# Kernel tuning notes

Measured on AMD Instinct MI355X. Metric: run time of the kernel, lower is better.

## Reference

```python
import jax, jax.numpy as jnp
import numpy as np

N = 50000      # nodes
E = 800000     # edges (before self-loops)
DIN = 128      # in_channels
DH = 64        # hidden_channels
HEADS = 2
DOUT = 64      # out_channels
NEG_SLOPE = 0.2  # PyG GATConv leaky_relu slope


def setup_inputs() -> dict:
    key = jax.random.key(0)
    ks = jax.random.split(key, 10)
    node_emb = jax.random.normal(ks[0], (N, DIN), dtype=jnp.float32)
    edge_index = jax.random.randint(ks[1], (2, E), 0, N, dtype=jnp.int64)
    # conv1: in -> hidden, heads=2, concat=True
    W1 = jax.random.normal(ks[2], (DIN, HEADS * DH), dtype=jnp.float32) / np.sqrt(DIN)
    att_src1 = jax.random.normal(ks[3], (HEADS, DH), dtype=jnp.float32) * 0.1
    att_dst1 = jax.random.normal(ks[4], (HEADS, DH), dtype=jnp.float32) * 0.1
    b1 = jnp.zeros((HEADS * DH,), dtype=jnp.float32)
    # conv2: hidden*heads -> out, heads=1, concat=False
    W2 = jax.random.normal(ks[5], (HEADS * DH, 1 * DOUT), dtype=jnp.float32) / np.sqrt(HEADS * DH)
    att_src2 = jax.random.normal(ks[6], (1, DOUT), dtype=jnp.float32) * 0.1
    att_dst2 = jax.random.normal(ks[7], (1, DOUT), dtype=jnp.float32) * 0.1
    b2 = jnp.zeros((DOUT,), dtype=jnp.float32)
    return {"node_emb": node_emb, "edge_index": edge_index,
            "W1": W1, "att_src1": att_src1, "att_dst1": att_dst1, "b1": b1,
            "W2": W2, "att_src2": att_src2, "att_dst2": att_dst2, "b2": b2}


def gat_layer(x, src, dst, W, att_src, att_dst, bias, heads, concat, n):
    # x: [N, Fin]; W: [Fin, heads*C]; att_*: [heads, C]
    C = W.shape[1] // heads
    h = (x @ W).reshape(n, heads, C)                       # [N, H, C]
    a_src = jnp.einsum('nhc,hc->nh', h, att_src)           # [N, H]
    a_dst = jnp.einsum('nhc,hc->nh', h, att_dst)           # [N, H]
    e = jax.nn.leaky_relu(a_src[src] + a_dst[dst], NEG_SLOPE)  # [E, H]
    # segment softmax over incoming edges of each destination node
    m = jax.ops.segment_max(e, dst, num_segments=n)        # [N, H]
    ex = jnp.exp(e - m[dst])
    denom = jax.ops.segment_sum(ex, dst, num_segments=n)   # [N, H]
    alpha = ex / denom[dst]                                # [E, H]
    out = jax.ops.segment_sum(h[src] * alpha[:, :, None], dst, num_segments=n)  # [N, H, C]
    if concat:
        out = out.reshape(n, heads * C)
    else:
        out = out.mean(axis=1)
    return out + bias


def reference(node_emb, edge_index, W1, att_src1, att_dst1, b1, W2, att_src2, att_dst2, b2):
    loops = jnp.arange(N, dtype=edge_index.dtype)
    src = jnp.concatenate([edge_index[0], loops])  # PyG add_self_loops=True
    dst = jnp.concatenate([edge_index[1], loops])
    h = gat_layer(node_emb, src, dst, W1, att_src1, att_dst1, b1, HEADS, True, N)
    h = jax.nn.elu(h)
    # dropout is identity in eval mode
    out = gat_layer(h, src, dst, W2, att_src2, att_dst2, b2, 1, False, N)
    return out
```

## Files before the change

kernel.cpp:

```cpp
#include <hip/hip_runtime.h>
#include <hip/hip_fp16.h>
#include <math.h>

constexpr float NEG_SLOPE = 0.2f;
constexpr int NPART = 8;
constexpr int WSLOT = 16;

__global__ void k_scatter(const int* __restrict__ src, const int* __restrict__ dst, int e,
                          int* __restrict__ cur, unsigned short* __restrict__ ell, int n) {
    int t = blockIdx.x * blockDim.x + threadIdx.x;
    int i0 = t * 4;
    int p = blockIdx.x & (NPART - 1);
    if (i0 + 3 < e) {
        int4 d4 = *reinterpret_cast<const int4*>(dst + i0);
        int4 s4 = *reinterpret_cast<const int4*>(src + i0);
        int a0 = atomicAdd(&cur[p * n + d4.x], 1);
        int a1 = atomicAdd(&cur[p * n + d4.y], 1);
        int a2 = atomicAdd(&cur[p * n + d4.z], 1);
        int a3 = atomicAdd(&cur[p * n + d4.w], 1);
        if (a0 < WSLOT) ell[((size_t)p * n + d4.x) * WSLOT + a0] = (unsigned short)s4.x;
        if (a1 < WSLOT) ell[((size_t)p * n + d4.y) * WSLOT + a1] = (unsigned short)s4.y;
        if (a2 < WSLOT) ell[((size_t)p * n + d4.z) * WSLOT + a2] = (unsigned short)s4.z;
        if (a3 < WSLOT) ell[((size_t)p * n + d4.w) * WSLOT + a3] = (unsigned short)s4.w;
    } else {
        for (int i = i0; i < e; i++) {
            int d = dst[i];
            int slot = atomicAdd(&cur[p * n + d], 1);
            if (slot < WSLOT) ell[((size_t)p * n + d) * WSLOT + slot] = (unsigned short)src[i];
        }
    }
}

__device__ inline __half2 u2h(unsigned int u) { return *reinterpret_cast<__half2*>(&u); }

__device__ inline void fmamix8(uint4 v, float al, float* acc) {
    float2 f0 = __half22float2(u2h(v.x)), f1 = __half22float2(u2h(v.y));
    float2 f2 = __half22float2(u2h(v.z)), f3 = __half22float2(u2h(v.w));
    acc[0] = fmaf(al, f0.x, acc[0]); acc[1] = fmaf(al, f0.y, acc[1]);
    acc[2] = fmaf(al, f1.x, acc[2]); acc[3] = fmaf(al, f1.y, acc[3]);
    acc[4] = fmaf(al, f2.x, acc[4]); acc[5] = fmaf(al, f2.y, acc[5]);
    acc[6] = fmaf(al, f3.x, acc[6]); acc[7] = fmaf(al, f3.y, acc[7]);
}

__device__ inline int ell_resolve(const unsigned short* __restrict__ ell,
                                  const int* pre, int node, int n, int l) {
    int p = 0;
#pragma unroll
    for (int t = 1; t < NPART; t++)
        if (l >= pre[t]) p = t;
    int slot = l - pre[p];
    return (int)ell[((size_t)p * n + node) * WSLOT + slot];
}

__global__ __launch_bounds__(256) void k_gemm1(const float* __restrict__ x,
                                               const float* __restrict__ W,
                                               const float* __restrict__ a_src,
                                               const float* __restrict__ a_dst,
                                               __half* __restrict__ h1h,
                                               float* __restrict__ att, int n) {
    __shared__ float xs[32 * 128];
    __shared__ float ws[128 * 128];
    int t = threadIdx.x;
    const float4* Wv = (const float4*)W;
    float4* wsv = (float4*)ws;
#pragma unroll
    for (int i = 0; i < 16; i++) wsv[t + 256 * i] = Wv[t + 256 * i];
    int row0 = blockIdx.x * 32;
    const float4* xv = (const float4*)x;
    float4* xsv = (float4*)xs;
#pragma unroll
    for (int ii = 0; ii < 4; ii++) {
        int i = t + 256 * ii;
        int r = i >> 5, c4 = i & 31;
        int gr = row0 + r;
        float4 v = (gr < n) ? xv[(size_t)gr * 32 + c4] : make_float4(0.f, 0.f, 0.f, 0.f);
        xsv[i] = v;
    }
    __syncthreads();
    int tc = t & 31;
    int tr = t >> 5;
    float acc[4][4];
#pragma unroll
    for (int i = 0; i < 4; i++)
#pragma unroll
        for (int j = 0; j < 4; j++) acc[i][j] = 0.f;
    const float4* wsv4 = (const float4*)ws;
    for (int k = 0; k < 128; k++) {
        float4 w4 = wsv4[k * 32 + tc];
#pragma unroll
        for (int i = 0; i < 4; i++) {
            float xvv = xs[(tr * 4 + i) * 128 + k];
            acc[i][0] = fmaf(xvv, w4.x, acc[i][0]);
            acc[i][1] = fmaf(xvv, w4.y, acc[i][1]);
            acc[i][2] = fmaf(xvv, w4.z, acc[i][2]);
            acc[i][3] = fmaf(xvv, w4.w, acc[i][3]);
        }
    }
#pragma unroll
    for (int i = 0; i < 4; i++) {
        int gr = row0 + tr * 4 + i;
        if (gr < n) {
            __half2 p01 = __floats2half2_rn(acc[i][0], acc[i][1]);
            __half2 p23 = __floats2half2_rn(acc[i][2], acc[i][3]);
            uint2 o;
            o.x = *reinterpret_cast<unsigned int*>(&p01);
            o.y = *reinterpret_cast<unsigned int*>(&p23);
            *reinterpret_cast<uint2*>(h1h + (size_t)gr * 128 + 4 * tc) = o;
        }
    }
    const float4* asv = (const float4*)a_src;
    const float4* adv = (const float4*)a_dst;
    float4 as4 = asv[tc], ad4 = adv[tc];
    int lane = t & 63;
#pragma unroll
    for (int i = 0; i < 4; i++) {
        float s = acc[i][0] * as4.x + acc[i][1] * as4.y + acc[i][2] * as4.z + acc[i][3] * as4.w;
        float d = acc[i][0] * ad4.x + acc[i][1] * ad4.y + acc[i][2] * ad4.z + acc[i][3] * ad4.w;
#pragma unroll
        for (int o = 1; o < 16; o <<= 1) {
            s += __shfl_xor(s, o);
            d += __shfl_xor(d, o);
        }
        float s1 = __shfl(s, (lane & 32) + 16);
        float d1 = __shfl(d, (lane & 32) + 16);
        int gr = row0 + tr * 4 + i;
        if ((lane & 31) == 0 && gr < n) {
            ((float4*)att)[gr] = make_float4(s, s1, d, d1);
        }
    }
}

__global__ __launch_bounds__(256) void k_gemm2(const float* __restrict__ x,
                                               const float* __restrict__ W,
                                               const float* __restrict__ a_src,
                                               const float* __restrict__ a_dst,
                                               __half* __restrict__ h2h,
                                               float* __restrict__ att, int n) {
    __shared__ float xs[32 * 128];
    __shared__ float ws[128 * 64];
    int t = threadIdx.x;
    const float4* Wv = (const float4*)W;
    float4* wsv = (float4*)ws;
#pragma unroll
    for (int i = 0; i < 8; i++) wsv[t + 256 * i] = Wv[t + 256 * i];
    int row0 = blockIdx.x * 32;
    const float4* xv = (const float4*)x;
    float4* xsv = (float4*)xs;
#pragma unroll
    for (int ii = 0; ii < 4; ii++) {
        int i = t + 256 * ii;
        int r = i >> 5, c4 = i & 31;
        int gr = row0 + r;
        float4 v = (gr < n) ? xv[(size_t)gr * 32 + c4] : make_float4(0.f, 0.f, 0.f, 0.f);
        xsv[i] = v;
    }
    __syncthreads();
    int tc = t & 15;
    int tr = t >> 4;
    float acc[2][4];
#pragma unroll
    for (int i = 0; i < 2; i++)
#pragma unroll
        for (int j = 0; j < 4; j++) acc[i][j] = 0.f;
    const float4* wsv4 = (const float4*)ws;
    for (int k = 0; k < 128; k++) {
        float4 w4 = wsv4[k * 16 + tc];
#pragma unroll
        for (int i = 0; i < 2; i++) {
            float xvv = xs[(tr * 2 + i) * 128 + k];
            acc[i][0] = fmaf(xvv, w4.x, acc[i][0]);
            acc[i][1] = fmaf(xvv, w4.y, acc[i][1]);
            acc[i][2] = fmaf(xvv, w4.z, acc[i][2]);
            acc[i][3] = fmaf(xvv, w4.w, acc[i][3]);
        }
    }
#pragma unroll
    for (int i = 0; i < 2; i++) {
        int gr = row0 + tr * 2 + i;
        if (gr < n) {
            __half2 p01 = __floats2half2_rn(acc[i][0], acc[i][1]);
            __half2 p23 = __floats2half2_rn(acc[i][2], acc[i][3]);
            uint2 o;
            o.x = *reinterpret_cast<unsigned int*>(&p01);
            o.y = *reinterpret_cast<unsigned int*>(&p23);
            *reinterpret_cast<uint2*>(h2h + (size_t)gr * 64 + 4 * tc) = o;
        }
    }
    const float4* asv = (const float4*)a_src;
    const float4* adv = (const float4*)a_dst;
    float4 as4 = asv[tc], ad4 = adv[tc];
#pragma unroll
    for (int i = 0; i < 2; i++) {
        float s = acc[i][0] * as4.x + acc[i][1] * as4.y + acc[i][2] * as4.z + acc[i][3] * as4.w;
        float d = acc[i][0] * ad4.x + acc[i][1] * ad4.y + acc[i][2] * ad4.z + acc[i][3] * ad4.w;
#pragma unroll
        for (int o = 1; o < 16; o <<= 1) {
            s += __shfl_xor(s, o);
            d += __shfl_xor(d, o);
        }
        int gr = row0 + tr * 2 + i;
        if (tc == 0 && gr < n) {
            ((float2*)att)[gr] = make_float2(s, d);
        }
    }
}

__global__ __launch_bounds__(256) void k_aggr1(const int* __restrict__ cur,
                                               const unsigned short* __restrict__ ell,
                                               const float* __restrict__ att,
                                               const __half* __restrict__ h1h,
                                               const float* __restrict__ bias,
                                               float* __restrict__ xout, int n) {
    int wid = threadIdx.x >> 6, lane = threadIdx.x & 63;
    int node = blockIdx.x * 4 + wid;
    if (node >= n) return;

    int cnt = 0;
    if (lane < NPART) cnt = cur[lane * n + node];
    int pre[NPART];
    int tot = 1;
#pragma unroll
    for (int p = 0; p < NPART; p++) {
        int cc = __shfl(cnt, p);
        cc = cc < WSLOT ? cc : WSLOT;
        pre[p] = tot;
        tot += cc;
    }

    const float4* attv = (const float4*)att;
    float4 an = attv[node];
    float ad0 = an.z, ad1 = an.w;

    int chq = lane & 15;
    int g = lane >> 4;
    bool hsel = (chq >= 8);

    float acc[8];
#pragma unroll
    for (int i = 0; i < 8; i++) acc[i] = 0.f;

    if (tot <= 64) {
        int c = node;
        float p0 = 0.f, p1 = 0.f;
        if (lane < tot) {
            if (lane > 0) c = ell_resolve(ell, pre, node, n, lane);
            float4 a = attv[c];
            float e0 = a.x + ad0; e0 = e0 > 0.f ? e0 : NEG_SLOPE * e0;
            float e1 = a.y + ad1; e1 = e1 > 0.f ? e1 : NEG_SLOPE * e1;
            p0 = __expf(e0); p1 = __expf(e1);
        }
        float sum0 = p0, sum1 = p1;
#pragma unroll
        for (int d = 1; d < 64; d <<= 1) {
            sum0 += __shfl_xor(sum0, d);
            sum1 += __shfl_xor(sum1, d);
        }
        float rsel = hsel ? (1.f / sum1) : (1.f / sum0);

        for (int k0 = 0; k0 < tot; k0 += 16) {
            uint4 v[4];
            float al[4];
#pragma unroll
            for (int u = 0; u < 4; u++) {
                int k = k0 + 4 * u + g;
                int ks = k & 63;
                int sn = __shfl(c, ks);
                float pa = __shfl(p0, ks);
                float pb = __shfl(p1, ks);
                al[u] = (k < tot) ? (hsel ? pb : pa) * rsel : 0.f;
                v[u] = *reinterpret_cast<const uint4*>(h1h + (size_t)sn * 128 + 8 * chq);
            }
#pragma unroll
            for (int u = 0; u < 4; u++) fmamix8(v[u], al[u], acc);
        }
    } else {
        float sum0 = 0.f, sum1 = 0.f;
        for (int l = lane; l < tot; l += 64) {
            int c = (l == 0) ? node : ell_resolve(ell, pre, node, n, l);
            float4 a = attv[c];
            float e0 = a.x + ad0; e0 = e0 > 0.f ? e0 : NEG_SLOPE * e0;
            float e1 = a.y + ad1; e1 = e1 > 0.f ? e1 : NEG_SLOPE * e1;
            sum0 += __expf(e0); sum1 += __expf(e1);
        }
#pragma unroll
        for (int d = 1; d < 64; d <<= 1) {
            sum0 += __shfl_xor(sum0, d);
            sum1 += __shfl_xor(sum1, d);
        }
        float rsel = hsel ? (1.f / sum1) : (1.f / sum0);
        for (int j = 0; j < tot; j += 4) {
            int l = j + g;
            bool valid = (l < tot);
            int lc = valid ? l : 0;
            int sn = (lc == 0) ? node : ell_resolve(ell, pre, node, n, lc);
            float4 a = attv[sn];
            float e0 = a.x + ad0; e0 = e0 > 0.f ? e0 : NEG_SLOPE * e0;
            float e1 = a.y + ad1; e1 = e1 > 0.f ? e1 : NEG_SLOPE * e1;
            float pp = hsel ? __expf(e1) : __expf(e0);
            float al = valid ? pp * rsel : 0.f;
            uint4 v = *reinterpret_cast<const uint4*>(h1h + (size_t)sn * 128 + 8 * chq);
            fmamix8(v, al, acc);
        }
    }

#pragma unroll
    for (int i = 0; i < 8; i++) {
        acc[i] += __shfl_xor(acc[i], 16);
        acc[i] += __shfl_xor(acc[i], 32);
    }
    if (lane < 16) {
        const float4* bv = (const float4*)bias;
        float4 bA = bv[2 * chq], bB = bv[2 * chq + 1];
        float o[8];
        o[0] = acc[0] + bA.x; o[1] = acc[1] + bA.y;
        o[2] = acc[2] + bA.z; o[3] = acc[3] + bA.w;
        o[4] = acc[4] + bB.x; o[5] = acc[5] + bB.y;
        o[6] = acc[6] + bB.z; o[7] = acc[7] + bB.w;
#pragma unroll
        for (int i = 0; i < 8; i++) o[i] = o[i] > 0.f ? o[i] : (__expf(o[i]) - 1.f);
        float4* ov = (float4*)(xout + (size_t)node * 128 + 8 * chq);
        ov[0] = make_float4(o[0], o[1], o[2], o[3]);
        ov[1] = make_float4(o[4], o[5], o[6], o[7]);
    }
}

__global__ __launch_bounds__(256) void k_aggr2(const int* __restrict__ cur,
                                               const unsigned short* __restrict__ ell,
                                               const float* __restrict__ att,
                                               const __half* __restrict__ h2h,
                                               const float* __restrict__ bias,
                                               float* __restrict__ out, int n) {
    int wid = threadIdx.x >> 6, lane = threadIdx.x & 63;
    int node = blockIdx.x * 4 + wid;
    if (node >= n) return;

    int cnt = 0;
    if (lane < NPART) cnt = cur[lane * n + node];
    int pre[NPART];
    int tot = 1;
#pragma unroll
    for (int p = 0; p < NPART; p++) {
        int cc = __shfl(cnt, p);
        cc = cc < WSLOT ? cc : WSLOT;
        pre[p] = tot;
        tot += cc;
    }

    const float2* attv = (const float2*)att;
    float adn = attv[node].y;
    int chq = lane & 7;
    int g = lane >> 3;

    float acc[8];
#pragma unroll
    for (int i = 0; i < 8; i++) acc[i] = 0.f;

    if (tot <= 64) {
        int c = node;
        float p = 0.f;
        if (lane < tot) {
            if (lane > 0) c = ell_resolve(ell, pre, node, n, lane);
            float e = attv[c].x + adn;
            e = e > 0.f ? e : NEG_SLOPE * e;
            p = __expf(e);
        }
        float sum = p;
#pragma unroll
        for (int d = 1; d < 64; d <<= 1) sum += __shfl_xor(sum, d);
        float r = 1.f / sum;

        for (int k0 = 0; k0 < tot; k0 += 16) {
            uint4 v[2];
            float al[2];
#pragma unroll
            for (int u = 0; u < 2; u++) {
                int k = k0 + 8 * u + g;
                int ks = k & 63;
                int sn = __shfl(c, ks);
                float pk = __shfl(p, ks);
                al[u] = (k < tot) ? pk * r : 0.f;
                v[u] = *reinterpret_cast<const uint4*>(h2h + (size_t)sn * 64 + 8 * chq);
            }
#pragma unroll
            for (int u = 0; u < 2; u++) {
                float2 f0 = __half22float2(u2h(v[u].x)), f1 = __half22float2(u2h(v[u].y));
                float2 f2 = __half22float2(u2h(v[u].z)), f3 = __half22float2(u2h(v[u].w));
                acc[0] = fmaf(al[u], f0.x, acc[0]); acc[1] = fmaf(al[u], f0.y, acc[1]);
                acc[2] = fmaf(al[u], f1.x, acc[2]); acc[3] = fmaf(al[u], f1.y, acc[3]);
                acc[4] = fmaf(al[u], f2.x, acc[4]); acc[5] = fmaf(al[u], f2.y, acc[5]);
                acc[6] = fmaf(al[u], f3.x, acc[6]); acc[7] = fmaf(al[u], f3.y, acc[7]);
            }
        }
    } else {
        float sum = 0.f;
        for (int l = lane; l < tot; l += 64) {
            int c = (l == 0) ? node : ell_resolve(ell, pre, node, n, l);
            float e = attv[c].x + adn;
            e = e > 0.f ? e : NEG_SLOPE * e;
            sum += __expf(e);
        }
#pragma unroll
        for (int d = 1; d < 64; d <<= 1) sum += __shfl_xor(sum, d);
        float r = 1.f / sum;
        for (int j = 0; j < tot; j += 8) {
            int l = j + g;
            bool valid = (l < tot);
            int lc = valid ? l : 0;
            int sn = (lc == 0) ? node : ell_resolve(ell, pre, node, n, lc);
            float e = attv[sn].x + adn;
            e = e > 0.f ? e : NEG_SLOPE * e;
            float al = valid ? __expf(e) * r : 0.f;
            uint4 v = *reinterpret_cast<const uint4*>(h2h + (size_t)sn * 64 + 8 * chq);
            fmamix8(v, al, acc);
        }
    }

#pragma unroll
    for (int i = 0; i < 8; i++) {
        acc[i] += __shfl_xor(acc[i], 8);
        acc[i] += __shfl_xor(acc[i], 16);
        acc[i] += __shfl_xor(acc[i], 32);
    }
    if (lane < 8) {
        const float4* bv = (const float4*)bias;
        float4 bA = bv[2 * chq], bB = bv[2 * chq + 1];
        float4* ov = (float4*)(out + (size_t)node * 64 + 8 * chq);
        ov[0] = make_float4(acc[0] + bA.x, acc[1] + bA.y, acc[2] + bA.z, acc[3] + bA.w);
        ov[1] = make_float4(acc[4] + bB.x, acc[5] + bB.y, acc[6] + bB.z, acc[7] + bB.w);
    }
}

extern "C" void kernel_launch(void* const* d_in, const int* in_sizes, int n_in,
                              void* d_out, int out_size, void* d_ws, size_t ws_size,
                              hipStream_t stream) {
    const float* x    = (const float*)d_in[0];
    const int*   ei   = (const int*)d_in[1];
    const float* W1   = (const float*)d_in[2];
    const float* asr1 = (const float*)d_in[3];
    const float* adt1 = (const float*)d_in[4];
    const float* b1   = (const float*)d_in[5];
    const float* W2   = (const float*)d_in[6];
    const float* asr2 = (const float*)d_in[7];
    const float* adt2 = (const float*)d_in[8];
    const float* b2   = (const float*)d_in[9];
    float* out = (float*)d_out;

    const int N = in_sizes[0] / 128;
    const int E = in_sizes[1] / 2;
    const int* srcI = ei;
    const int* dstI = ei + E;

    char* p = (char*)d_ws;
    auto alloc = [&](size_t b) -> void* {
        void* r = (void*)p;
        p += ((b + 255) / 256) * 256;
        return r;
    };
    int* cur = (int*)alloc(sizeof(int) * (size_t)NPART * N);
    unsigned short* ell = (unsigned short*)alloc(sizeof(unsigned short) *
                                                 (size_t)NPART * N * WSLOT);
    __half* h1h = (__half*)alloc(sizeof(__half) * (size_t)N * 128);
    float* att1 = (float*)alloc(sizeof(float) * (size_t)N * 4);
    float* x2   = (float*)alloc(sizeof(float) * (size_t)N * 128);
    __half* h2h = (__half*)alloc(sizeof(__half) * (size_t)N * 64);
    float* att2 = (float*)alloc(sizeof(float) * (size_t)N * 2);

    int nbE4 = (E + 1023) / 1024;
    int nbNode4 = (N + 3) / 4;
    int nbRow32 = (N + 31) / 32;

    hipMemsetAsync(cur, 0, sizeof(int) * (size_t)NPART * N, stream);
    k_scatter<<<nbE4, 256, 0, stream>>>(srcI, dstI, E, cur, ell, N);

    k_gemm1<<<nbRow32, 256, 0, stream>>>(x, W1, asr1, adt1, h1h, att1, N);
    k_aggr1<<<nbNode4, 256, 0, stream>>>(cur, ell, att1, h1h, b1, x2, N);

    k_gemm2<<<nbRow32, 256, 0, stream>>>(x2, W2, asr2, adt2, h2h, att2, N);
    k_aggr2<<<nbNode4, 256, 0, stream>>>(cur, ell, att2, h2h, b2, out, N);
}
```

Measured before the change: 171.1 us.

## Fuse scatter into gemm1, use half weights, half x2, and half2 aggregation

Merges the edge-scatter kernel and the first GEMM into one launch, interleaving scatter blocks with GEMM blocks so the atomic scatter overlaps the compute. The GEMM weights are stored in shared memory as fp16, which halves LDS use and should allow more resident blocks. The layer-1 output x2 is written as fp16, halving its write and re-read traffic. Both aggregation fast paths accumulate with packed half2 FMAs instead of fp32, which risks extra rounding error and overflow in the accumulators.

```diff
diff --git a/kernel.cpp b/kernel.cpp
--- a/kernel.cpp
+++ b/kernel.cpp
@@ -6,32 +6,8 @@
 constexpr int NPART = 8;
 constexpr int WSLOT = 16;
 
-__global__ void k_scatter(const int* __restrict__ src, const int* __restrict__ dst, int e,
-                          int* __restrict__ cur, unsigned short* __restrict__ ell, int n) {
-    int t = blockIdx.x * blockDim.x + threadIdx.x;
-    int i0 = t * 4;
-    int p = blockIdx.x & (NPART - 1);
-    if (i0 + 3 < e) {
-        int4 d4 = *reinterpret_cast<const int4*>(dst + i0);
-        int4 s4 = *reinterpret_cast<const int4*>(src + i0);
-        int a0 = atomicAdd(&cur[p * n + d4.x], 1);
-        int a1 = atomicAdd(&cur[p * n + d4.y], 1);
-        int a2 = atomicAdd(&cur[p * n + d4.z], 1);
-        int a3 = atomicAdd(&cur[p * n + d4.w], 1);
-        if (a0 < WSLOT) ell[((size_t)p * n + d4.x) * WSLOT + a0] = (unsigned short)s4.x;
-        if (a1 < WSLOT) ell[((size_t)p * n + d4.y) * WSLOT + a1] = (unsigned short)s4.y;
-        if (a2 < WSLOT) ell[((size_t)p * n + d4.z) * WSLOT + a2] = (unsigned short)s4.z;
-        if (a3 < WSLOT) ell[((size_t)p * n + d4.w) * WSLOT + a3] = (unsigned short)s4.w;
-    } else {
-        for (int i = i0; i < e; i++) {
-            int d = dst[i];
-            int slot = atomicAdd(&cur[p * n + d], 1);
-            if (slot < WSLOT) ell[((size_t)p * n + d) * WSLOT + slot] = (unsigned short)src[i];
-        }
-    }
-}
-
 __device__ inline __half2 u2h(unsigned int u) { return *reinterpret_cast<__half2*>(&u); }
+__device__ inline unsigned int h2u(__half2 h) { return *reinterpret_cast<unsigned int*>(&h); }
 
 __device__ inline void fmamix8(uint4 v, float al, float* acc) {
     float2 f0 = __half22float2(u2h(v.x)), f1 = __half22float2(u2h(v.y));
@@ -52,20 +28,58 @@
     return (int)ell[((size_t)p * n + node) * WSLOT + slot];
 }
 
-__global__ __launch_bounds__(256) void k_gemm1(const float* __restrict__ x,
-                                               const float* __restrict__ W,
-                                               const float* __restrict__ a_src,
-                                               const float* __restrict__ a_dst,
-                                               __half* __restrict__ h1h,
-                                               float* __restrict__ att, int n) {
+__global__ __launch_bounds__(256) void k_fused1(
+    const int* __restrict__ src, const int* __restrict__ dst, int e, int S, int G,
+    int* __restrict__ cur, unsigned short* __restrict__ ell,
+    const float* __restrict__ x, const float* __restrict__ W,
+    const float* __restrict__ a_src, const float* __restrict__ a_dst,
+    __half* __restrict__ h1h, float* __restrict__ att, int n) {
     __shared__ float xs[32 * 128];
-    __shared__ float ws[128 * 128];
+    __shared__ __half wsh[128 * 128];
+    int bid = blockIdx.x;
     int t = threadIdx.x;
+
+    int third = bid / 3;
+    bool interleave = (2 * S <= G + 2);
+    bool isScat = interleave ? ((bid % 3 == 0) && (third < S)) : (bid < S);
+    if (isScat) {
+        int sid = interleave ? third : bid;
+        int p = bid & (NPART - 1);
+        int i0 = (sid * 256 + t) * 4;
+        if (i0 + 3 < e) {
+            int4 d4 = *reinterpret_cast<const int4*>(dst + i0);
+            int4 s4 = *reinterpret_cast<const int4*>(src + i0);
+            int a0 = atomicAdd(&cur[p * n + d4.x], 1);
+            int a1 = atomicAdd(&cur[p * n + d4.y], 1);
+            int a2 = atomicAdd(&cur[p * n + d4.z], 1);
+            int a3 = atomicAdd(&cur[p * n + d4.w], 1);
+            if (a0 < WSLOT) ell[((size_t)p * n + d4.x) * WSLOT + a0] = (unsigned short)s4.x;
+            if (a1 < WSLOT) ell[((size_t)p * n + d4.y) * WSLOT + a1] = (unsigned short)s4.y;
+            if (a2 < WSLOT) ell[((size_t)p * n + d4.z) * WSLOT + a2] = (unsigned short)s4.z;
+            if (a3 < WSLOT) ell[((size_t)p * n + d4.w) * WSLOT + a3] = (unsigned short)s4.w;
+        } else {
+            for (int i = i0; i < e; i++) {
+                int d = dst[i];
+                int slot = atomicAdd(&cur[p * n + d], 1);
+                if (slot < WSLOT) ell[((size_t)p * n + d) * WSLOT + slot] = (unsigned short)src[i];
+            }
+        }
+        return;
+    }
+    int gid = interleave ? (bid - min(S, (bid + 2) / 3)) : (bid - S);
+    if (gid >= G) return;
+
     const float4* Wv = (const float4*)W;
-    float4* wsv = (float4*)ws;
-#pragma unroll
-    for (int i = 0; i < 16; i++) wsv[t + 256 * i] = Wv[t + 256 * i];
-    int row0 = blockIdx.x * 32;
+    uint2* wsv = (uint2*)wsh;
+#pragma unroll
+    for (int i = 0; i < 16; i++) {
+        float4 w = Wv[t + 256 * i];
+        __half2 a = __floats2half2_rn(w.x, w.y);
+        __half2 b = __floats2half2_rn(w.z, w.w);
+        uint2 o; o.x = h2u(a); o.y = h2u(b);
+        wsv[t + 256 * i] = o;
+    }
+    int row0 = gid * 32;
     const float4* xv = (const float4*)x;
     float4* xsv = (float4*)xs;
 #pragma unroll
@@ -84,16 +98,18 @@
     for (int i = 0; i < 4; i++)
 #pragma unroll
         for (int j = 0; j < 4; j++) acc[i][j] = 0.f;
-    const float4* wsv4 = (const float4*)ws;
+    const uint2* wsv2 = (const uint2*)wsh;
     for (int k = 0; k < 128; k++) {
-        float4 w4 = wsv4[k * 32 + tc];
+        uint2 wu = wsv2[k * 32 + tc];
+        float2 wA = __half22float2(u2h(wu.x));
+        float2 wB = __half22float2(u2h(wu.y));
 #pragma unroll
         for (int i = 0; i < 4; i++) {
             float xvv = xs[(tr * 4 + i) * 128 + k];
-            acc[i][0] = fmaf(xvv, w4.x, acc[i][0]);
-            acc[i][1] = fmaf(xvv, w4.y, acc[i][1]);
-            acc[i][2] = fmaf(xvv, w4.z, acc[i][2]);
-            acc[i][3] = fmaf(xvv, w4.w, acc[i][3]);
+            acc[i][0] = fmaf(xvv, wA.x, acc[i][0]);
+            acc[i][1] = fmaf(xvv, wA.y, acc[i][1]);
+            acc[i][2] = fmaf(xvv, wB.x, acc[i][2]);
+            acc[i][3] = fmaf(xvv, wB.y, acc[i][3]);
         }
     }
 #pragma unroll
@@ -102,9 +118,7 @@
         if (gr < n) {
             __half2 p01 = __floats2half2_rn(acc[i][0], acc[i][1]);
             __half2 p23 = __floats2half2_rn(acc[i][2], acc[i][3]);
-            uint2 o;
-            o.x = *reinterpret_cast<unsigned int*>(&p01);
-            o.y = *reinterpret_cast<unsigned int*>(&p23);
+            uint2 o; o.x = h2u(p01); o.y = h2u(p23);
             *reinterpret_cast<uint2*>(h1h + (size_t)gr * 128 + 4 * tc) = o;
         }
     }
@@ -130,29 +144,36 @@
     }
 }
 
-__global__ __launch_bounds__(256) void k_gemm2(const float* __restrict__ x,
+__global__ __launch_bounds__(256) void k_gemm2(const __half* __restrict__ x2h,
                                                const float* __restrict__ W,
                                                const float* __restrict__ a_src,
                                                const float* __restrict__ a_dst,
                                                __half* __restrict__ h2h,
                                                float* __restrict__ att, int n) {
     __shared__ float xs[32 * 128];
-    __shared__ float ws[128 * 64];
+    __shared__ __half wsh[128 * 64];
     int t = threadIdx.x;
     const float4* Wv = (const float4*)W;
-    float4* wsv = (float4*)ws;
-#pragma unroll
-    for (int i = 0; i < 8; i++) wsv[t + 256 * i] = Wv[t + 256 * i];
+    uint2* wsv = (uint2*)wsh;
+#pragma unroll
+    for (int i = 0; i < 8; i++) {
+        float4 w = Wv[t + 256 * i];
+        __half2 a = __floats2half2_rn(w.x, w.y);
+        __half2 b = __floats2half2_rn(w.z, w.w);
+        uint2 o; o.x = h2u(a); o.y = h2u(b);
+        wsv[t + 256 * i] = o;
+    }
     int row0 = blockIdx.x * 32;
-    const float4* xv = (const float4*)x;
+    const uint2* xv = (const uint2*)x2h;
     float4* xsv = (float4*)xs;
 #pragma unroll
     for (int ii = 0; ii < 4; ii++) {
         int i = t + 256 * ii;
         int r = i >> 5, c4 = i & 31;
         int gr = row0 + r;
-        float4 v = (gr < n) ? xv[(size_t)gr * 32 + c4] : make_float4(0.f, 0.f, 0.f, 0.f);
-        xsv[i] = v;
+        uint2 u = (gr < n) ? xv[(size_t)gr * 32 + c4] : make_uint2(0u, 0u);
+        float2 lo = __half22float2(u2h(u.x)), hi = __half22float2(u2h(u.y));
+        xsv[i] = make_float4(lo.x, lo.y, hi.x, hi.y);
     }
     __syncthreads();
     int tc = t & 15;
@@ -162,16 +183,18 @@
     for (int i = 0; i < 2; i++)
 #pragma unroll
         for (int j = 0; j < 4; j++) acc[i][j] = 0.f;
-    const float4* wsv4 = (const float4*)ws;
+    const uint2* wsv2 = (const uint2*)wsh;
     for (int k = 0; k < 128; k++) {
-        float4 w4 = wsv4[k * 16 + tc];
+        uint2 wu = wsv2[k * 16 + tc];
+        float2 wA = __half22float2(u2h(wu.x));
+        float2 wB = __half22float2(u2h(wu.y));
 #pragma unroll
         for (int i = 0; i < 2; i++) {
             float xvv = xs[(tr * 2 + i) * 128 + k];
-            acc[i][0] = fmaf(xvv, w4.x, acc[i][0]);
-            acc[i][1] = fmaf(xvv, w4.y, acc[i][1]);
-            acc[i][2] = fmaf(xvv, w4.z, acc[i][2]);
-            acc[i][3] = fmaf(xvv, w4.w, acc[i][3]);
+            acc[i][0] = fmaf(xvv, wA.x, acc[i][0]);
+            acc[i][1] = fmaf(xvv, wA.y, acc[i][1]);
+            acc[i][2] = fmaf(xvv, wB.x, acc[i][2]);
+            acc[i][3] = fmaf(xvv, wB.y, acc[i][3]);
         }
     }
 #pragma unroll
@@ -180,9 +203,7 @@
         if (gr < n) {
             __half2 p01 = __floats2half2_rn(acc[i][0], acc[i][1]);
             __half2 p23 = __floats2half2_rn(acc[i][2], acc[i][3]);
-            uint2 o;
-            o.x = *reinterpret_cast<unsigned int*>(&p01);
-            o.y = *reinterpret_cast<unsigned int*>(&p23);
+            uint2 o; o.x = h2u(p01); o.y = h2u(p23);
             *reinterpret_cast<uint2*>(h2h + (size_t)gr * 64 + 4 * tc) = o;
         }
     }
@@ -210,7 +231,7 @@
                                                const float* __restrict__ att,
                                                const __half* __restrict__ h1h,
                                                const float* __restrict__ bias,
-                                               float* __restrict__ xout, int n) {
+                                               __half* __restrict__ x2h, int n) {
     int wid = threadIdx.x >> 6, lane = threadIdx.x & 63;
     int node = blockIdx.x * 4 + wid;
     if (node >= n) return;
@@ -235,9 +256,7 @@
     int g = lane >> 4;
     bool hsel = (chq >= 8);
 
-    float acc[8];
-#pragma unroll
-    for (int i = 0; i < 8; i++) acc[i] = 0.f;
+    float f[8];
 
     if (tot <= 64) {
         int c = node;
@@ -257,9 +276,11 @@
         }
         float rsel = hsel ? (1.f / sum1) : (1.f / sum0);
 
+        __half2 z = __float2half2_rn(0.f);
+        __half2 hacc0 = z, hacc1 = z, hacc2 = z, hacc3 = z;
         for (int k0 = 0; k0 < tot; k0 += 16) {
             uint4 v[4];
-            float al[4];
+            __half2 al2[4];
 #pragma unroll
             for (int u = 0; u < 4; u++) {
                 int k = k0 + 4 * u + g;
@@ -267,12 +288,22 @@
                 int sn = __shfl(c, ks);
                 float pa = __shfl(p0, ks);
                 float pb = __shfl(p1, ks);
-                al[u] = (k < tot) ? (hsel ? pb : pa) * rsel : 0.f;
+                float alf = (k < tot) ? (hsel ? pb : pa) * rsel : 0.f;
+                al2[u] = __float2half2_rn(alf);
                 v[u] = *reinterpret_cast<const uint4*>(h1h + (size_t)sn * 128 + 8 * chq);
             }
 #pragma unroll
-            for (int u = 0; u < 4; u++) fmamix8(v[u], al[u], acc);
-        }
+            for (int u = 0; u < 4; u++) {
+                hacc0 = __hfma2(al2[u], u2h(v[u].x), hacc0);
+                hacc1 = __hfma2(al2[u], u2h(v[u].y), hacc1);
+                hacc2 = __hfma2(al2[u], u2h(v[u].z), hacc2);
+                hacc3 = __hfma2(al2[u], u2h(v[u].w), hacc3);
+            }
+        }
+        f[0] = __low2float(hacc0); f[1] = __high2float(hacc0);
+        f[2] = __low2float(hacc1); f[3] = __high2float(hacc1);
+        f[4] = __low2float(hacc2); f[5] = __high2float(hacc2);
+        f[6] = __low2float(hacc3); f[7] = __high2float(hacc3);
     } else {
         float sum0 = 0.f, sum1 = 0.f;
         for (int l = lane; l < tot; l += 64) {
@@ -288,6 +319,9 @@
             sum1 += __shfl_xor(sum1, d);
         }
         float rsel = hsel ? (1.f / sum1) : (1.f / sum0);
+        float acc[8];
+#pragma unroll
+        for (int i = 0; i < 8; i++) acc[i] = 0.f;
         for (int j = 0; j < tot; j += 4) {
             int l = j + g;
             bool valid = (l < tot);
@@ -301,26 +335,31 @@
             uint4 v = *reinterpret_cast<const uint4*>(h1h + (size_t)sn * 128 + 8 * chq);
             fmamix8(v, al, acc);
         }
+#pragma unroll
+        for (int i = 0; i < 8; i++) f[i] = acc[i];
     }
 
 #pragma unroll
     for (int i = 0; i < 8; i++) {
-        acc[i] += __shfl_xor(acc[i], 16);
-        acc[i] += __shfl_xor(acc[i], 32);
+        f[i] += __shfl_xor(f[i], 16);
+        f[i] += __shfl_xor(f[i], 32);
     }
     if (lane < 16) {
         const float4* bv = (const float4*)bias;
         float4 bA = bv[2 * chq], bB = bv[2 * chq + 1];
         float o[8];
-        o[0] = acc[0] + bA.x; o[1] = acc[1] + bA.y;
-        o[2] = acc[2] + bA.z; o[3] = acc[3] + bA.w;
-        o[4] = acc[4] + bB.x; o[5] = acc[5] + bB.y;
-        o[6] = acc[6] + bB.z; o[7] = acc[7] + bB.w;
+        o[0] = f[0] + bA.x; o[1] = f[1] + bA.y;
+        o[2] = f[2] + bA.z; o[3] = f[3] + bA.w;
+        o[4] = f[4] + bB.x; o[5] = f[5] + bB.y;
+        o[6] = f[6] + bB.z; o[7] = f[7] + bB.w;
 #pragma unroll
         for (int i = 0; i < 8; i++) o[i] = o[i] > 0.f ? o[i] : (__expf(o[i]) - 1.f);
-        float4* ov = (float4*)(xout + (size_t)node * 128 + 8 * chq);
-        ov[0] = make_float4(o[0], o[1], o[2], o[3]);
-        ov[1] = make_float4(o[4], o[5], o[6], o[7]);
+        __half2 q01 = __floats2half2_rn(o[0], o[1]);
+        __half2 q23 = __floats2half2_rn(o[2], o[3]);
+        __half2 q45 = __floats2half2_rn(o[4], o[5]);
+        __half2 q67 = __floats2half2_rn(o[6], o[7]);
+        uint4 w; w.x = h2u(q01); w.y = h2u(q23); w.z = h2u(q45); w.w = h2u(q67);
+        *reinterpret_cast<uint4*>(x2h + (size_t)node * 128 + 8 * chq) = w;
     }
 }
 
@@ -351,9 +390,7 @@
     int chq = lane & 7;
     int g = lane >> 3;
 
-    float acc[8];
-#pragma unroll
-    for (int i = 0; i < 8; i++) acc[i] = 0.f;
+    float f[8];
 
     if (tot <= 64) {
         int c = node;
@@ -369,28 +406,33 @@
         for (int d = 1; d < 64; d <<= 1) sum += __shfl_xor(sum, d);
         float r = 1.f / sum;
 
+        __half2 z = __float2half2_rn(0.f);
+        __half2 hacc0 = z, hacc1 = z, hacc2 = z, hacc3 = z;
         for (int k0 = 0; k0 < tot; k0 += 16) {
             uint4 v[2];
-            float al[2];
+            __half2 al2[2];
 #pragma unroll
             for (int u = 0; u < 2; u++) {
                 int k = k0 + 8 * u + g;
                 int ks = k & 63;
                 int sn = __shfl(c, ks);
                 float pk = __shfl(p, ks);
-                al[u] = (k < tot) ? pk * r : 0.f;
+                float alf = (k < tot) ? pk * r : 0.f;
+                al2[u] = __float2half2_rn(alf);
                 v[u] = *reinterpret_cast<const uint4*>(h2h + (size_t)sn * 64 + 8 * chq);
             }
 #pragma unroll
             for (int u = 0; u < 2; u++) {
-                float2 f0 = __half22float2(u2h(v[u].x)), f1 = __half22float2(u2h(v[u].y));
-                float2 f2 = __half22float2(u2h(v[u].z)), f3 = __half22float2(u2h(v[u].w));
-                acc[0] = fmaf(al[u], f0.x, acc[0]); acc[1] = fmaf(al[u], f0.y, acc[1]);
-                acc[2] = fmaf(al[u], f1.x, acc[2]); acc[3] = fmaf(al[u], f1.y, acc[3]);
-                acc[4] = fmaf(al[u], f2.x, acc[4]); acc[5] = fmaf(al[u], f2.y, acc[5]);
-                acc[6] = fmaf(al[u], f3.x, acc[6]); acc[7] = fmaf(al[u], f3.y, acc[7]);
+                hacc0 = __hfma2(al2[u], u2h(v[u].x), hacc0);
+                hacc1 = __hfma2(al2[u], u2h(v[u].y), hacc1);
+                hacc2 = __hfma2(al2[u], u2h(v[u].z), hacc2);
+                hacc3 = __hfma2(al2[u], u2h(v[u].w), hacc3);
             }
         }
+        f[0] = __low2float(hacc0); f[1] = __high2float(hacc0);
+        f[2] = __low2float(hacc1); f[3] = __high2float(hacc1);
+        f[4] = __low2float(hacc2); f[5] = __high2float(hacc2);
+        f[6] = __low2float(hacc3); f[7] = __high2float(hacc3);
     } else {
         float sum = 0.f;
         for (int l = lane; l < tot; l += 64) {
@@ -402,6 +444,9 @@
 #pragma unroll
         for (int d = 1; d < 64; d <<= 1) sum += __shfl_xor(sum, d);
         float r = 1.f / sum;
+        float acc[8];
+#pragma unroll
+        for (int i = 0; i < 8; i++) acc[i] = 0.f;
         for (int j = 0; j < tot; j += 8) {
             int l = j + g;
             bool valid = (l < tot);
@@ -413,20 +458,22 @@
             uint4 v = *reinterpret_cast<const uint4*>(h2h + (size_t)sn * 64 + 8 * chq);
             fmamix8(v, al, acc);
         }
+#pragma unroll
+        for (int i = 0; i < 8; i++) f[i] = acc[i];
     }
 
 #pragma unroll
     for (int i = 0; i < 8; i++) {
-        acc[i] += __shfl_xor(acc[i], 8);
-        acc[i] += __shfl_xor(acc[i], 16);
-        acc[i] += __shfl_xor(acc[i], 32);
+        f[i] += __shfl_xor(f[i], 8);
+        f[i] += __shfl_xor(f[i], 16);
+        f[i] += __shfl_xor(f[i], 32);
     }
     if (lane < 8) {
         const float4* bv = (const float4*)bias;
         float4 bA = bv[2 * chq], bB = bv[2 * chq + 1];
         float4* ov = (float4*)(out + (size_t)node * 64 + 8 * chq);
-        ov[0] = make_float4(acc[0] + bA.x, acc[1] + bA.y, acc[2] + bA.z, acc[3] + bA.w);
-        ov[1] = make_float4(acc[4] + bB.x, acc[5] + bB.y, acc[6] + bB.z, acc[7] + bB.w);
+        ov[0] = make_float4(f[0] + bA.x, f[1] + bA.y, f[2] + bA.z, f[3] + bA.w);
+        ov[1] = make_float4(f[4] + bB.x, f[5] + bB.y, f[6] + bB.z, f[7] + bB.w);
     }
 }
 
@@ -461,20 +508,22 @@
                                                  (size_t)NPART * N * WSLOT);
     __half* h1h = (__half*)alloc(sizeof(__half) * (size_t)N * 128);
     float* att1 = (float*)alloc(sizeof(float) * (size_t)N * 4);
-    float* x2   = (float*)alloc(sizeof(float) * (size_t)N * 128);
+    __half* x2h = (__half*)alloc(sizeof(__half) * (size_t)N * 128);
     __half* h2h = (__half*)alloc(sizeof(__half) * (size_t)N * 64);
     float* att2 = (float*)alloc(sizeof(float) * (size_t)N * 2);
 
-    int nbE4 = (E + 1023) / 1024;
+    int S = (E + 1023) / 1024;
+    int G = (N + 31) / 32;
     int nbNode4 = (N + 3) / 4;
     int nbRow32 = (N + 31) / 32;
 
     hipMemsetAsync(cur, 0, sizeof(int) * (size_t)NPART * N, stream);
-    k_scatter<<<nbE4, 256, 0, stream>>>(srcI, dstI, E, cur, ell, N);
-
-    k_gemm1<<<nbRow32, 256, 0, stream>>>(x, W1, asr1, adt1, h1h, att1, N);
-    k_aggr1<<<nbNode4, 256, 0, stream>>>(cur, ell, att1, h1h, b1, x2, N);
-
-    k_gemm2<<<nbRow32, 256, 0, stream>>>(x2, W2, asr2, adt2, h2h, att2, N);
+
+    k_fused1<<<S + G, 256, 0, stream>>>(srcI, dstI, E, S, G, cur, ell,
+                                        x, W1, asr1, adt1, h1h, att1, N);
+
+    k_aggr1<<<nbNode4, 256, 0, stream>>>(cur, ell, att1, h1h, b1, x2h, N);
+
+    k_gemm2<<<nbRow32, 256, 0, stream>>>(x2h, W2, asr2, adt2, h2h, att2, N);
     k_aggr2<<<nbNode4, 256, 0, stream>>>(cur, ell, att2, h2h, b2, out, N);
 }
```

Result: faster. 146.3 us (-14.5%).
